# Optimization experiments

Measured on AMD Instinct MI355X. Metric: run time of the kernel, lower is better.

Reference implementation:

```python
import jax, jax.numpy as jnp
import numpy as np

B, N, F_IN, F_OUT = 8, 2048, 128, 128


def setup_inputs() -> dict:
    key = jax.random.key(0)
    k1, k2, k3, k4 = jax.random.split(key, 4)
    stdv = 1.0 / np.sqrt(F_OUT)
    X = jax.random.normal(k1, (B, N, F_IN), dtype=jnp.float32)
    adj = jax.random.uniform(k2, (B, N, N), dtype=jnp.float32)
    W = jax.random.uniform(k3, (F_IN, F_OUT), minval=-stdv, maxval=stdv, dtype=jnp.float32)
    b = jax.random.uniform(k4, (F_OUT,), minval=-stdv, maxval=stdv, dtype=jnp.float32)
    return {"X": X, "adj": adj, "W": W, "b": b}


def reference(X, adj, W, b):
    # XW: [B, N, F_out]
    XW = jnp.einsum('bnf,fo->bno', X, W)
    # adj + I (self loops)
    adj = adj + jnp.eye(adj.shape[1], dtype=adj.dtype)[None]
    # symmetric degree normalization: D^-1/2 A D^-1/2, done as row/col scaling
    d = jnp.sum(adj, axis=-1)                 # [B, N]
    r = d ** -0.5                             # [B, N]
    adj = adj * r[:, :, None] * r[:, None, :] # [B, N, N]
    y = jnp.einsum('bnm,bmo->bno', adj, XW) + b
    return jax.nn.leaky_relu(y, negative_slope=0.01)
```

## Files before the change

kernel.cpp:

```cpp
#include <hip/hip_runtime.h>
#include <hip/hip_bf16.h>

#define BB 8
#define NN 2048
#define FD 128

typedef float f32x4 __attribute__((ext_vector_type(4)));
typedef short bf16x8 __attribute__((ext_vector_type(8)));
typedef short s16x4 __attribute__((ext_vector_type(4)));

__device__ __forceinline__ short f2bf(float f) {
  union { __hip_bfloat16 h; short s; } u;
  u.h = __float2bfloat16(f);
  return u.s;
}

__global__ __launch_bounds__(256) void k_xw_fused(const float* __restrict__ X,
                                                  const float* __restrict__ adj,
                                                  const float* __restrict__ W,
                                                  short* __restrict__ bpack,
                                                  float* __restrict__ xwsr,
                                                  float* __restrict__ r) {
  __shared__ __align__(16) float Xs[64][132];
  __shared__ __align__(16) float Ws[128][128];
  __shared__ float Ls[64];
  const int b    = blockIdx.y;
  const int m0   = blockIdx.x * 64;
  const int t    = threadIdx.x;
  const int lane = t & 63;
  const int w    = t >> 6;

  {
    const float* base = adj + ((size_t)b * NN + m0 + w * 16) * NN;
    for (int rr = 0; rr < 16; ++rr) {
      const f32x4* p = reinterpret_cast<const f32x4*>(base + (size_t)rr * NN);
      float s = 0.f;
#pragma unroll
      for (int i = 0; i < 8; ++i) {
        f32x4 v = p[lane + 64 * i];
        s += (v.x + v.y) + (v.z + v.w);
      }
#pragma unroll
      for (int off = 32; off >= 1; off >>= 1) s += __shfl_xor(s, off, 64);
      if (lane == 0) {
        float rv = rsqrtf(1.0f + s);
        Ls[w * 16 + rr] = rv;
        r[b * NN + m0 + w * 16 + rr] = rv;
      }
    }
  }
  {
    const f32x4* wp = reinterpret_cast<const f32x4*>(W);
    f32x4* wd = reinterpret_cast<f32x4*>(&Ws[0][0]);
#pragma unroll
    for (int i = 0; i < 16; ++i) wd[t + 256 * i] = wp[t + 256 * i];
    const f32x4* xp = reinterpret_cast<const f32x4*>(X + ((size_t)b * NN + m0) * FD);
#pragma unroll
    for (int i = 0; i < 8; ++i) {
      int slot = t + 256 * i;
      f32x4 v = xp[slot];
      *reinterpret_cast<f32x4*>(&Xs[slot >> 5][(slot & 31) * 4]) = v;
    }
  }
  __syncthreads();

  const int ot = (t & 15) * 8;
  const int mt = (t >> 4) * 4;
  float acc[4][8];
#pragma unroll
  for (int i = 0; i < 4; ++i)
#pragma unroll
    for (int j = 0; j < 8; ++j) acc[i][j] = 0.f;

  for (int k = 0; k < 128; k += 4) {
    f32x4 xv[4];
#pragma unroll
    for (int i = 0; i < 4; ++i) xv[i] = *reinterpret_cast<const f32x4*>(&Xs[mt + i][k]);
#pragma unroll
    for (int kk = 0; kk < 4; ++kk) {
      float wv[8];
#pragma unroll
      for (int j = 0; j < 8; ++j) wv[j] = Ws[k + kk][ot + j];
#pragma unroll
      for (int i = 0; i < 4; ++i)
#pragma unroll
        for (int j = 0; j < 8; ++j) acc[i][j] = fmaf(xv[i][kk], wv[j], acc[i][j]);
    }
  }
  const int bm = b * NN + m0 + mt;
#pragma unroll
  for (int i = 0; i < 4; ++i) {
    float rm = Ls[mt + i];
#pragma unroll
    for (int j = 0; j < 8; ++j) acc[i][j] *= rm;
  }
#pragma unroll
  for (int i = 0; i < 4; ++i) {
    f32x4 lo = {acc[i][0], acc[i][1], acc[i][2], acc[i][3]};
    f32x4 hi = {acc[i][4], acc[i][5], acc[i][6], acc[i][7]};
    float* dst = xwsr + (size_t)(bm + i) * FD + ot;
    *reinterpret_cast<f32x4*>(dst) = lo;
    *reinterpret_cast<f32x4*>(dst + 4) = hi;
  }
  short* bp = bpack + (size_t)b * NN * FD;
  const int grp = (m0 + mt) >> 3;
  const int h   = ((m0 + mt) >> 2) & 1;
#pragma unroll
  for (int j = 0; j < 8; ++j) {
    s16x4 sv;
#pragma unroll
    for (int i = 0; i < 4; ++i) sv[i] = f2bf(acc[i][j]);
    *reinterpret_cast<s16x4*>(bp + (size_t)grp * 1024 + (ot + j) * 8 + h * 4) = sv;
  }
}

__global__ __launch_bounds__(256) void k_gemm2(const float* __restrict__ adj,
                                               const short* __restrict__ bpack,
                                               const float* __restrict__ xwsr,
                                               const float* __restrict__ r,
                                               const float* __restrict__ bias,
                                               float* __restrict__ out) {
  const int b    = blockIdx.y;
  const int n0   = blockIdx.x * 64;
  const int t    = threadIdx.x;
  const int lane = t & 63;
  const int w    = t >> 6;
  const int rowloc = w * 16 + (lane & 15);
  const float* ap  = adj + ((size_t)b * NN + n0 + rowloc) * NN + (lane >> 4) * 8;
  const short* bpb = bpack + (size_t)b * NN * FD + (size_t)(lane >> 4) * 1024 + (lane & 15) * 8;

  f32x4 acc[8];
#pragma unroll
  for (int i = 0; i < 8; ++i) acc[i] = (f32x4){0.f, 0.f, 0.f, 0.f};

  f32x4 aA[2], aB[2];
  bf16x8 bA[8], bB[8];

  auto loadA = [&](int ks, f32x4 (&d)[2]) {
    const f32x4* p = reinterpret_cast<const f32x4*>(ap + ks * 32);
    d[0] = p[0];
    d[1] = p[1];
  };
  auto loadB = [&](int ks, bf16x8 (&d)[8]) {
    const short* p = bpb + (size_t)ks * 4096;
#pragma unroll
    for (int ct = 0; ct < 8; ++ct)
      d[ct] = *reinterpret_cast<const bf16x8*>(p + ct * 128);
  };
  auto step = [&](f32x4 (&sa)[2], bf16x8 (&sb)[8]) {
    bf16x8 af;
#pragma unroll
    for (int i = 0; i < 4; ++i) { af[i] = f2bf(sa[0][i]); af[4 + i] = f2bf(sa[1][i]); }
#pragma unroll
    for (int ct = 0; ct < 8; ++ct)
      acc[ct] = __builtin_amdgcn_mfma_f32_16x16x32_bf16(af, sb[ct], acc[ct], 0, 0, 0);
  };

  loadA(0, aA); loadB(0, bA);
  loadA(1, aB); loadB(1, bB);
  for (int ks = 0; ks < 64; ks += 2) {
    step(aA, bA);
    if (ks + 2 < 64) { loadA(ks + 2, aA); loadB(ks + 2, bA); }
    step(aB, bB);
    if (ks + 3 < 64) { loadA(ks + 3, aB); loadB(ks + 3, bB); }
  }

  const int col = lane & 15, rq = lane >> 4;
  const float* xr = xwsr + ((size_t)b * NN + n0 + w * 16) * FD;
  float* ob = out + ((size_t)b * NN + n0 + w * 16) * FD;
#pragma unroll
  for (int reg = 0; reg < 4; ++reg) {
    const int rloc = rq * 4 + reg;
    const float rn = r[b * NN + n0 + w * 16 + rloc];
#pragma unroll
    for (int ct = 0; ct < 8; ++ct) {
      const int o = ct * 16 + col;
      float v = acc[ct][reg] + xr[(size_t)rloc * FD + o];
      v = rn * v + bias[o];
      ob[(size_t)rloc * FD + o] = v > 0.f ? v : 0.01f * v;
    }
  }
}

extern "C" void kernel_launch(void* const* d_in, const int* in_sizes, int n_in,
                              void* d_out, int out_size, void* d_ws, size_t ws_size,
                              hipStream_t stream) {
  (void)in_sizes; (void)n_in; (void)out_size; (void)ws_size;
  const float* X    = (const float*)d_in[0];
  const float* adj  = (const float*)d_in[1];
  const float* W    = (const float*)d_in[2];
  const float* bias = (const float*)d_in[3];
  float* out = (float*)d_out;

  char* ws = (char*)d_ws;
  float* r     = (float*)ws;
  short* bpack = (short*)(ws + 65536);
  float* xwsr  = (float*)(ws + 65536 + (size_t)BB * NN * FD * 2);

  k_xw_fused<<<dim3(NN / 64, BB), dim3(256), 0, stream>>>(X, adj, W, bpack, xwsr, r);
  k_gemm2<<<dim3(NN / 64, BB), dim3(256), 0, stream>>>(adj, bpack, xwsr, r, bias, out);
}
```

Before: 72.12 us.

## Split-K gemm2 across waves with LDS reduction, deeper prefetch, batched row sums

In the second GEMM, each block now covers 32 rows instead of 64. Two wave pairs each handle half of K, and their partial results are combined through shared memory before the epilogue. This doubles the grid and the number of concurrent adj streams. A 4-deep A prefetch and s_setprio around the MFMAs are also added. The first kernel issues its W and X loads early and batches the 16 row-sum reductions to expose more memory parallelism, at the cost of higher register pressure.

```diff
diff --git a/kernel.cpp b/kernel.cpp
--- a/kernel.cpp
+++ b/kernel.cpp
@@ -30,36 +30,50 @@
   const int lane = t & 63;
   const int w    = t >> 6;
 
+  f32x4 wreg[16], xreg[8];
   {
+    const f32x4* wp = reinterpret_cast<const f32x4*>(W);
+#pragma unroll
+    for (int i = 0; i < 16; ++i) wreg[i] = wp[t + 256 * i];
+    const f32x4* xp = reinterpret_cast<const f32x4*>(X + ((size_t)b * NN + m0) * FD);
+#pragma unroll
+    for (int i = 0; i < 8; ++i) xreg[i] = xp[t + 256 * i];
+  }
+
+  {
+    float s[16];
+#pragma unroll
+    for (int rr = 0; rr < 16; ++rr) s[rr] = 0.f;
     const float* base = adj + ((size_t)b * NN + m0 + w * 16) * NN;
+#pragma unroll
     for (int rr = 0; rr < 16; ++rr) {
       const f32x4* p = reinterpret_cast<const f32x4*>(base + (size_t)rr * NN);
-      float s = 0.f;
 #pragma unroll
       for (int i = 0; i < 8; ++i) {
         f32x4 v = p[lane + 64 * i];
-        s += (v.x + v.y) + (v.z + v.w);
+        s[rr] += (v.x + v.y) + (v.z + v.w);
       }
-#pragma unroll
-      for (int off = 32; off >= 1; off >>= 1) s += __shfl_xor(s, off, 64);
+    }
+#pragma unroll
+    for (int rr = 0; rr < 16; ++rr) {
+      float v = s[rr];
+#pragma unroll
+      for (int off = 32; off >= 1; off >>= 1) v += __shfl_xor(v, off, 64);
       if (lane == 0) {
-        float rv = rsqrtf(1.0f + s);
+        float rv = rsqrtf(1.0f + v);
         Ls[w * 16 + rr] = rv;
         r[b * NN + m0 + w * 16 + rr] = rv;
       }
     }
   }
   {
-    const f32x4* wp = reinterpret_cast<const f32x4*>(W);
     f32x4* wd = reinterpret_cast<f32x4*>(&Ws[0][0]);
 #pragma unroll
-    for (int i = 0; i < 16; ++i) wd[t + 256 * i] = wp[t + 256 * i];
-    const f32x4* xp = reinterpret_cast<const f32x4*>(X + ((size_t)b * NN + m0) * FD);
+    for (int i = 0; i < 16; ++i) wd[t + 256 * i] = wreg[i];
 #pragma unroll
     for (int i = 0; i < 8; ++i) {
       int slot = t + 256 * i;
-      f32x4 v = xp[slot];
-      *reinterpret_cast<f32x4*>(&Xs[slot >> 5][(slot & 31) * 4]) = v;
+      *reinterpret_cast<f32x4*>(&Xs[slot >> 5][(slot & 31) * 4]) = xreg[i];
     }
   }
   __syncthreads();
@@ -120,26 +134,30 @@
                                                const float* __restrict__ r,
                                                const float* __restrict__ bias,
                                                float* __restrict__ out) {
-  const int b    = blockIdx.y;
-  const int n0   = blockIdx.x * 64;
-  const int t    = threadIdx.x;
-  const int lane = t & 63;
-  const int w    = t >> 6;
-  const int rowloc = w * 16 + (lane & 15);
-  const float* ap  = adj + ((size_t)b * NN + n0 + rowloc) * NN + (lane >> 4) * 8;
-  const short* bpb = bpack + (size_t)b * NN * FD + (size_t)(lane >> 4) * 1024 + (lane & 15) * 8;
+  __shared__ float Red[2][16][128];
+  const int b     = blockIdx.y;
+  const int n0    = blockIdx.x * 32;
+  const int t     = threadIdx.x;
+  const int lane  = t & 63;
+  const int w     = t >> 6;
+  const int strip = w & 1;
+  const int khalf = w >> 1;
+  const int rowb  = n0 + strip * 16;
+
+  const float* ap  = adj + ((size_t)b * NN + rowb + (lane & 15)) * NN + khalf * 1024 + (lane >> 4) * 8;
+  const short* bpb = bpack + (size_t)b * NN * FD + (size_t)(khalf * 128 + (lane >> 4)) * 1024 + (lane & 15) * 8;
 
   f32x4 acc[8];
 #pragma unroll
   for (int i = 0; i < 8; ++i) acc[i] = (f32x4){0.f, 0.f, 0.f, 0.f};
 
-  f32x4 aA[2], aB[2];
-  bf16x8 bA[8], bB[8];
+  f32x4 aS[4][2];
+  bf16x8 bS[2][8];
 
   auto loadA = [&](int ks, f32x4 (&d)[2]) {
-    const f32x4* p = reinterpret_cast<const f32x4*>(ap + ks * 32);
-    d[0] = p[0];
-    d[1] = p[1];
+    const f32x4* q = reinterpret_cast<const f32x4*>(ap + ks * 32);
+    d[0] = q[0];
+    d[1] = q[1];
   };
   auto loadB = [&](int ks, bf16x8 (&d)[8]) {
     const short* p = bpb + (size_t)ks * 4096;
@@ -151,33 +169,45 @@
     bf16x8 af;
 #pragma unroll
     for (int i = 0; i < 4; ++i) { af[i] = f2bf(sa[0][i]); af[4 + i] = f2bf(sa[1][i]); }
+    __builtin_amdgcn_s_setprio(1);
 #pragma unroll
     for (int ct = 0; ct < 8; ++ct)
       acc[ct] = __builtin_amdgcn_mfma_f32_16x16x32_bf16(af, sb[ct], acc[ct], 0, 0, 0);
+    __builtin_amdgcn_s_setprio(0);
   };
 
-  loadA(0, aA); loadB(0, bA);
-  loadA(1, aB); loadB(1, bB);
-  for (int ks = 0; ks < 64; ks += 2) {
-    step(aA, bA);
-    if (ks + 2 < 64) { loadA(ks + 2, aA); loadB(ks + 2, bA); }
-    step(aB, bB);
-    if (ks + 3 < 64) { loadA(ks + 3, aB); loadB(ks + 3, bB); }
+  loadA(0, aS[0]); loadA(1, aS[1]); loadA(2, aS[2]); loadA(3, aS[3]);
+  loadB(0, bS[0]); loadB(1, bS[1]);
+#pragma unroll
+  for (int ks = 0; ks < 32; ++ks) {
+    step(aS[ks & 3], bS[ks & 1]);
+    if (ks + 4 < 32) loadA(ks + 4, aS[ks & 3]);
+    if (ks + 2 < 32) loadB(ks + 2, bS[ks & 1]);
   }
 
   const int col = lane & 15, rq = lane >> 4;
-  const float* xr = xwsr + ((size_t)b * NN + n0 + w * 16) * FD;
-  float* ob = out + ((size_t)b * NN + n0 + w * 16) * FD;
-#pragma unroll
-  for (int reg = 0; reg < 4; ++reg) {
-    const int rloc = rq * 4 + reg;
-    const float rn = r[b * NN + n0 + w * 16 + rloc];
-#pragma unroll
-    for (int ct = 0; ct < 8; ++ct) {
-      const int o = ct * 16 + col;
-      float v = acc[ct][reg] + xr[(size_t)rloc * FD + o];
-      v = rn * v + bias[o];
-      ob[(size_t)rloc * FD + o] = v > 0.f ? v : 0.01f * v;
+  if (khalf == 1) {
+#pragma unroll
+    for (int reg = 0; reg < 4; ++reg)
+#pragma unroll
+      for (int ct = 0; ct < 8; ++ct)
+        Red[strip][rq * 4 + reg][ct * 16 + col] = acc[ct][reg];
+  }
+  __syncthreads();
+  if (khalf == 0) {
+    const float* xr = xwsr + ((size_t)b * NN + rowb) * FD;
+    float* ob = out + ((size_t)b * NN + rowb) * FD;
+#pragma unroll
+    for (int reg = 0; reg < 4; ++reg) {
+      const int rloc = rq * 4 + reg;
+      const float rn = r[b * NN + rowb + rloc];
+#pragma unroll
+      for (int ct = 0; ct < 8; ++ct) {
+        const int o = ct * 16 + col;
+        float v = acc[ct][reg] + Red[strip][rloc][o] + xr[(size_t)rloc * FD + o];
+        v = rn * v + bias[o];
+        ob[(size_t)rloc * FD + o] = v > 0.f ? v : 0.01f * v;
+      }
     }
   }
 }
@@ -198,5 +228,5 @@
   float* xwsr  = (float*)(ws + 65536 + (size_t)BB * NN * FD * 2);
 
   k_xw_fused<<<dim3(NN / 64, BB), dim3(256), 0, stream>>>(X, adj, W, bpack, xwsr, r);
-  k_gemm2<<<dim3(NN / 64, BB), dim3(256), 0, stream>>>(adj, bpack, xwsr, r, bias, out);
-}
+  k_gemm2<<<dim3(NN / 32, BB), dim3(256), 0, stream>>>(adj, bpack, xwsr, r, bias, out);
+}
```

Measured after the change: 93.85 us. +30.1%, slower.
